# Kernel tuning notes

Hardware: AMD Instinct MI355X
Metric: run time of the kernel (lower is better)

## Reference

```python
import jax, jax.numpy as jnp
import numpy as np

EPS = 1e-12


def setup_inputs() -> dict:
    key = jax.random.key(0)
    N, C, H, W = 32, 256, 56, 56
    k1, k2, k3 = jax.random.split(key, 3)
    x = jax.random.normal(k1, (N, C, H, W), dtype=jnp.float32)
    weight = 1.0 + 0.1 * jax.random.normal(k2, (C,), dtype=jnp.float32)
    bias = 0.1 * jax.random.normal(k3, (C,), dtype=jnp.float32)
    # Variable group sizes summing to C=256 (16 groups)
    gs = np.array([8, 24, 8, 16, 32, 16, 8, 8, 16, 24, 8, 16, 16, 8, 32, 16], dtype=np.int64)
    assert gs.sum() == C
    # Per-sample channel permutation expressed as row indices into x.view(N*C, H*W)
    rng = np.random.default_rng(0)
    perms = np.stack([rng.permutation(C) for _ in range(N)])  # [N, C]
    offs = np.arange(N)[:, None] * C
    indexes = (perms + offs).reshape(-1).astype(np.int64)
    inv = np.argsort(perms, axis=1)
    reverse_indexes = (inv + offs).reshape(-1).astype(np.int64)
    return {
        "x": x,
        "weight": weight,
        "bias": bias,
        "group_sizes": jnp.asarray(gs),
        "indexes": jnp.asarray(indexes),
        "reverse_indexes": jnp.asarray(reverse_indexes),
    }


def reference(x, weight, bias, group_sizes, indexes, reverse_indexes):
    N, C, H, W = x.shape
    HW = H * W
    gs = np.asarray(group_sizes)          # static group layout
    G = gs.shape[0]
    seg = jnp.asarray(np.repeat(np.arange(G), gs))  # [C] channel -> group id
    n = jnp.asarray(gs * HW, dtype=x.dtype)         # [G] elements per group

    # gather: per-sample channel permutation
    xg = x.reshape(N * C, HW)[indexes].reshape(N, C, HW)

    # per-group mean via segmented reduction over channels
    s1 = xg.sum(axis=2)                                    # [N, C]
    mu_g = jax.ops.segment_sum(s1.T, seg, num_segments=G).T / n      # [N, G]
    mu_c = mu_g[:, seg]                                    # [N, C]

    diff = xg - mu_c[:, :, None]
    s2 = (diff * diff).sum(axis=2)                         # [N, C]
    # torch.var default is unbiased -> divide by (n - 1)
    var_g = jax.ops.segment_sum(s2.T, seg, num_segments=G).T / (n - 1.0)
    ivar_c = (1.0 / jnp.sqrt(var_g + EPS))[:, seg]         # [N, C]

    out = diff * ivar_c[:, :, None] * weight[None, :, None] + bias[None, :, None]

    # scatter back to original channel order
    out = out.reshape(N * C, HW)[reverse_indexes].reshape(N, C, H, W)
    return out
```

## Files before the change

### kernel.cpp

```cpp
#include <hip/hip_runtime.h>

#define N_ 32
#define C_ 256
#define G_ 16
#define HW_ 3136
#define HW4_ 784
#define NBIN_ 8
#define BLK_ 1024
#define NWAVE_ (BLK_ / 64)
#define EPS_ 1e-12f

typedef float vf4 __attribute__((ext_vector_type(4)));

__device__ __forceinline__ int rd_int(const int* __restrict__ p, int i, bool is64) {
    return is64 ? p[2 * i] : p[i];
}

__global__ __launch_bounds__(BLK_) void vgn_fused(
    const float* __restrict__ x,
    const int*   __restrict__ indexes,
    const int*   __restrict__ group_sizes,
    const float* __restrict__ weight,
    const float* __restrict__ bias,
    float*       __restrict__ out)
{
    const bool is64 = (group_sizes[1] == 0);
    const int n   = blockIdx.x >> 3;
    const int bin = blockIdx.x & (NBIN_ - 1);
    const int tid = threadIdx.x;

    __shared__ int   sGs[G_], sPg[G_];
    __shared__ int   sOrd[G_], sLoad[NBIN_];
    __shared__ int   sGrpId[G_];
    __shared__ int   sGrpStart[G_ + 1];
    __shared__ int   sGrpCnt, sNRows;
    __shared__ int   sRowSrc[C_];
    __shared__ float sRowScale[C_], sRowShift[C_];
    __shared__ float sMu[G_], sIvar[G_];
    __shared__ float sRed[2 * NWAVE_];

    if (tid == 0) {
        int P = 0;
        for (int k = 0; k < G_; k++) {
            int g = rd_int(group_sizes, k, is64);
            sGs[k] = g; sPg[k] = P; P += g;
            sOrd[k] = k;
        }
        for (int a = 0; a < G_; a++) {
            int best = a;
            for (int b = a + 1; b < G_; b++)
                if (sGs[sOrd[b]] > sGs[sOrd[best]]) best = b;
            int t = sOrd[a]; sOrd[a] = sOrd[best]; sOrd[best] = t;
        }
        for (int b = 0; b < NBIN_; b++) sLoad[b] = 0;
        int cnt = 0, rows = 0;
        for (int a = 0; a < G_; a++) {
            int bmin = 0;
            for (int b = 1; b < NBIN_; b++) if (sLoad[b] < sLoad[bmin]) bmin = b;
            int gid = sOrd[a];
            if (bmin == bin) {
                sGrpId[cnt]    = gid;
                sGrpStart[cnt] = rows;
                rows += sGs[gid];
                cnt++;
            }
            sLoad[bmin] += sGs[gid];
        }
        sGrpStart[cnt] = rows;
        sGrpCnt = cnt;
        sNRows  = rows;
    }
    __syncthreads();

    const int nGrp  = sGrpCnt;
    const int nRows = sNRows;

    if (tid < nRows) {
        int a = 0;
        while (!(tid >= sGrpStart[a] && tid < sGrpStart[a + 1])) a++;
        int j = sPg[sGrpId[a]] + (tid - sGrpStart[a]);
        sRowSrc[tid] = rd_int(indexes, n * C_ + j, is64);
    }
    __syncthreads();

    const int wave = tid >> 6;
    const int lane = tid & 63;

    for (int a = 0; a < nGrp; a++) {
        const int r0  = sGrpStart[a];
        const int gsz = sGrpStart[a + 1] - r0;
        const int tot = gsz * HW4_;
        float s = 0.f, s2 = 0.f;
        for (int idx = tid; idx < tot; idx += BLK_) {
            int r   = idx / HW4_;
            int col = idx - r * HW4_;
            const vf4* p = (const vf4*)(x + (size_t)sRowSrc[r0 + r] * HW_);
            vf4 v = p[col];
            s += v.x + v.y + v.z + v.w;
            s2 = fmaf(v.x, v.x, s2);
            s2 = fmaf(v.y, v.y, s2);
            s2 = fmaf(v.z, v.z, s2);
            s2 = fmaf(v.w, v.w, s2);
        }
        #pragma unroll
        for (int off = 32; off > 0; off >>= 1) {
            s  += __shfl_down(s,  off);
            s2 += __shfl_down(s2, off);
        }
        if (lane == 0) { sRed[wave] = s; sRed[NWAVE_ + wave] = s2; }
        __syncthreads();
        if (tid == 0) {
            float S = 0.f, S2 = 0.f;
            for (int w = 0; w < NWAVE_; w++) { S += sRed[w]; S2 += sRed[NWAVE_ + w]; }
            float cnt = (float)gsz * (float)HW_;
            float mu  = S / cnt;
            float var = (S2 - mu * S) / (cnt - 1.0f);
            sMu[a]   = mu;
            sIvar[a] = rsqrtf(var + EPS_);
        }
        __syncthreads();
    }

    if (tid < nRows) {
        int a = 0;
        while (!(tid >= sGrpStart[a] && tid < sGrpStart[a + 1])) a++;
        int j = sPg[sGrpId[a]] + (tid - sGrpStart[a]);
        float sc = sIvar[a] * weight[j];
        sRowScale[tid] = sc;
        sRowShift[tid] = fmaf(-sMu[a], sc, bias[j]);
    }
    __syncthreads();

    const int tot = nRows * HW4_;
    for (int idx = tid; idx < tot; idx += BLK_) {
        int r   = idx / HW4_;
        int col = idx - r * HW4_;
        const size_t base = (size_t)sRowSrc[r] * HW4_;
        vf4 v = ((const vf4*)x)[base + col];
        float sc = sRowScale[r], sh = sRowShift[r];
        vf4 o;
        o.x = fmaf(v.x, sc, sh);
        o.y = fmaf(v.y, sc, sh);
        o.z = fmaf(v.z, sc, sh);
        o.w = fmaf(v.w, sc, sh);
        __builtin_nontemporal_store(o, (vf4*)out + base + col);
    }
}

extern "C" void kernel_launch(void* const* d_in, const int* in_sizes, int n_in,
                              void* d_out, int out_size, void* d_ws, size_t ws_size,
                              hipStream_t stream) {
    const float* x           = (const float*)d_in[0];
    const float* weight      = (const float*)d_in[1];
    const float* bias        = (const float*)d_in[2];
    const int*   group_sizes = (const int*)  d_in[3];
    const int*   indexes     = (const int*)  d_in[4];

    dim3 grid(N_ * NBIN_), block(BLK_);
    vgn_fused<<<grid, block, 0, stream>>>(x, indexes, group_sizes,
                                          weight, bias, (float*)d_out);
}
```

Before: 216.3 us.

## Assign rows to half-wave teams and reduce per row instead of per group

Each 32-lane team now owns whole rows in both the statistics and normalize passes, using fixed-trip unrolled loops over the 784 vec4 columns. This removes the per-element integer division and the two block-wide barriers per group. Per-row partial sums are written to shared memory and a few threads combine them per group after a single barrier. The trade-off is less even load balance when nRows is not a multiple of 32, and a 16-lane tail that leaves half the lanes idle.

Result: no change. 214.6 us (-0.8%).

```diff
diff --git a/kernel.cpp b/kernel.cpp
--- a/kernel.cpp
+++ b/kernel.cpp
@@ -7,7 +7,6 @@
 #define HW4_ 784
 #define NBIN_ 8
 #define BLK_ 1024
-#define NWAVE_ (BLK_ / 64)
 #define EPS_ 1e-12f
 
 typedef float vf4 __attribute__((ext_vector_type(4)));
@@ -35,9 +34,9 @@
     __shared__ int   sGrpStart[G_ + 1];
     __shared__ int   sGrpCnt, sNRows;
     __shared__ int   sRowSrc[C_];
+    __shared__ float sRowS[C_], sRowS2[C_];
     __shared__ float sRowScale[C_], sRowShift[C_];
     __shared__ float sMu[G_], sIvar[G_];
-    __shared__ float sRed[2 * NWAVE_];
 
     if (tid == 0) {
         int P = 0;
@@ -77,53 +76,59 @@
 
     if (tid < nRows) {
         int a = 0;
-        while (!(tid >= sGrpStart[a] && tid < sGrpStart[a + 1])) a++;
+        while (tid >= sGrpStart[a + 1]) a++;
         int j = sPg[sGrpId[a]] + (tid - sGrpStart[a]);
         sRowSrc[tid] = rd_int(indexes, n * C_ + j, is64);
     }
     __syncthreads();
 
-    const int wave = tid >> 6;
-    const int lane = tid & 63;
+    const int rowT   = tid >> 5;
+    const int lane32 = tid & 31;
 
-    for (int a = 0; a < nGrp; a++) {
-        const int r0  = sGrpStart[a];
-        const int gsz = sGrpStart[a + 1] - r0;
-        const int tot = gsz * HW4_;
+    for (int r = rowT; r < nRows; r += 32) {
+        const vf4* p4 = (const vf4*)(x + (size_t)sRowSrc[r] * HW_);
         float s = 0.f, s2 = 0.f;
-        for (int idx = tid; idx < tot; idx += BLK_) {
-            int r   = idx / HW4_;
-            int col = idx - r * HW4_;
-            const vf4* p = (const vf4*)(x + (size_t)sRowSrc[r0 + r] * HW_);
-            vf4 v = p[col];
-            s += v.x + v.y + v.z + v.w;
-            s2 = fmaf(v.x, v.x, s2);
-            s2 = fmaf(v.y, v.y, s2);
-            s2 = fmaf(v.z, v.z, s2);
-            s2 = fmaf(v.w, v.w, s2);
+        #pragma unroll 8
+        for (int it = 0; it < 24; ++it) {
+            vf4 v = p4[lane32 + (it << 5)];
+            s  += v.x + v.y + v.z + v.w;
+            s2  = fmaf(v.x, v.x, s2);
+            s2  = fmaf(v.y, v.y, s2);
+            s2  = fmaf(v.z, v.z, s2);
+            s2  = fmaf(v.w, v.w, s2);
+        }
+        if (lane32 < 16) {
+            vf4 v = p4[768 + lane32];
+            s  += v.x + v.y + v.z + v.w;
+            s2  = fmaf(v.x, v.x, s2);
+            s2  = fmaf(v.y, v.y, s2);
+            s2  = fmaf(v.z, v.z, s2);
+            s2  = fmaf(v.w, v.w, s2);
         }
         #pragma unroll
-        for (int off = 32; off > 0; off >>= 1) {
+        for (int off = 16; off > 0; off >>= 1) {
             s  += __shfl_down(s,  off);
             s2 += __shfl_down(s2, off);
         }
-        if (lane == 0) { sRed[wave] = s; sRed[NWAVE_ + wave] = s2; }
-        __syncthreads();
-        if (tid == 0) {
-            float S = 0.f, S2 = 0.f;
-            for (int w = 0; w < NWAVE_; w++) { S += sRed[w]; S2 += sRed[NWAVE_ + w]; }
-            float cnt = (float)gsz * (float)HW_;
-            float mu  = S / cnt;
-            float var = (S2 - mu * S) / (cnt - 1.0f);
-            sMu[a]   = mu;
-            sIvar[a] = rsqrtf(var + EPS_);
-        }
-        __syncthreads();
+        if (lane32 == 0) { sRowS[r] = s; sRowS2[r] = s2; }
     }
+    __syncthreads();
+
+    if (tid < nGrp) {
+        float S = 0.f, S2 = 0.f;
+        const int r0 = sGrpStart[tid], r1 = sGrpStart[tid + 1];
+        for (int r = r0; r < r1; r++) { S += sRowS[r]; S2 += sRowS2[r]; }
+        const float cnt = (float)(r1 - r0) * (float)HW_;
+        const float mu  = S / cnt;
+        const float var = (S2 - mu * S) / (cnt - 1.0f);
+        sMu[tid]   = mu;
+        sIvar[tid] = rsqrtf(var + EPS_);
+    }
+    __syncthreads();
 
     if (tid < nRows) {
         int a = 0;
-        while (!(tid >= sGrpStart[a] && tid < sGrpStart[a + 1])) a++;
+        while (tid >= sGrpStart[a + 1]) a++;
         int j = sPg[sGrpId[a]] + (tid - sGrpStart[a]);
         float sc = sIvar[a] * weight[j];
         sRowScale[tid] = sc;
@@ -131,19 +136,32 @@
     }
     __syncthreads();
 
-    const int tot = nRows * HW4_;
-    for (int idx = tid; idx < tot; idx += BLK_) {
-        int r   = idx / HW4_;
-        int col = idx - r * HW4_;
+    for (int r = rowT; r < nRows; r += 32) {
         const size_t base = (size_t)sRowSrc[r] * HW4_;
-        vf4 v = ((const vf4*)x)[base + col];
-        float sc = sRowScale[r], sh = sRowShift[r];
-        vf4 o;
-        o.x = fmaf(v.x, sc, sh);
-        o.y = fmaf(v.y, sc, sh);
-        o.z = fmaf(v.z, sc, sh);
-        o.w = fmaf(v.w, sc, sh);
-        __builtin_nontemporal_store(o, (vf4*)out + base + col);
+        const vf4* p4 = (const vf4*)x + base;
+        vf4*       o4 = (vf4*)out     + base;
+        const float sc = sRowScale[r], sh = sRowShift[r];
+        #pragma unroll 8
+        for (int it = 0; it < 24; ++it) {
+            const int i = lane32 + (it << 5);
+            vf4 v = p4[i];
+            vf4 o;
+            o.x = fmaf(v.x, sc, sh);
+            o.y = fmaf(v.y, sc, sh);
+            o.z = fmaf(v.z, sc, sh);
+            o.w = fmaf(v.w, sc, sh);
+            __builtin_nontemporal_store(o, o4 + i);
+        }
+        if (lane32 < 16) {
+            const int i = 768 + lane32;
+            vf4 v = p4[i];
+            vf4 o;
+            o.x = fmaf(v.x, sc, sh);
+            o.y = fmaf(v.y, sc, sh);
+            o.z = fmaf(v.z, sc, sh);
+            o.w = fmaf(v.w, sc, sh);
+            __builtin_nontemporal_store(o, o4 + i);
+        }
     }
 }
 
```

## Split fused group-norm into per-row reduce and normalize kernels

Applied to the files above, without the earlier changes.

Replaces the single fused kernel, which used 256 large blocks each handling a bin of groups, with two kernels over 4096 small blocks of two rows each. The first kernel writes per-row sum and sum-of-squares to workspace. The second combines those per group with a warp shuffle and applies the affine transform. The aim is far more parallelism and less serialized group looping. In exchange, x is read twice from memory rather than partly from cache, and there is an extra launch and a dependency through workspace.

After: 202.3 us. 6.5% less time.

```diff
diff --git a/kernel.cpp b/kernel.cpp
--- a/kernel.cpp
+++ b/kernel.cpp
@@ -5,145 +5,152 @@
 #define G_ 16
 #define HW_ 3136
 #define HW4_ 784
-#define NBIN_ 8
-#define BLK_ 1024
-#define NWAVE_ (BLK_ / 64)
 #define EPS_ 1e-12f
 
 typedef float vf4 __attribute__((ext_vector_type(4)));
+typedef float vf2 __attribute__((ext_vector_type(2)));
 
 __device__ __forceinline__ int rd_int(const int* __restrict__ p, int i, bool is64) {
     return is64 ? p[2 * i] : p[i];
 }
 
-__global__ __launch_bounds__(BLK_) void vgn_fused(
+__device__ __forceinline__ void acc4(const vf4 v, float& s, float& s2) {
+    s += v.x + v.y + v.z + v.w;
+    s2 = fmaf(v.x, v.x, s2);
+    s2 = fmaf(v.y, v.y, s2);
+    s2 = fmaf(v.z, v.z, s2);
+    s2 = fmaf(v.w, v.w, s2);
+}
+
+__device__ __forceinline__ vf4 aff(const vf4 v, float sc, float sh) {
+    vf4 r;
+    r.x = fmaf(v.x, sc, sh);
+    r.y = fmaf(v.y, sc, sh);
+    r.z = fmaf(v.z, sc, sh);
+    r.w = fmaf(v.w, sc, sh);
+    return r;
+}
+
+
+__global__ __launch_bounds__(256, 8) void vgn_reduce(
+    const float* __restrict__ x,
+    const int*   __restrict__ indexes,
+    const int*   __restrict__ group_sizes,
+    float*       __restrict__ rsums)
+{
+    const bool is64 = (group_sizes[1] == 0);
+    const int t  = threadIdx.x;
+    const int r0 = blockIdx.x * 2;
+
+    const int src0 = rd_int(indexes, r0,     is64);
+    const int src1 = rd_int(indexes, r0 + 1, is64);
+    const vf4* p0 = (const vf4*)x + (size_t)src0 * HW4_;
+    const vf4* p1 = (const vf4*)x + (size_t)src1 * HW4_;
+
+    vf4 a0 = p0[t], b0 = p0[t + 256], c0 = p0[t + 512];
+    vf4 a1 = p1[t], b1 = p1[t + 256], c1 = p1[t + 512];
+
+    float sA = 0.f, qA = 0.f, sB = 0.f, qB = 0.f;
+    if (t < 16) {
+        vf4 d0 = p0[768 + t];
+        vf4 d1 = p1[768 + t];
+        acc4(d0, sA, qA);
+        acc4(d1, sB, qB);
+    }
+    acc4(a0, sA, qA); acc4(b0, sA, qA); acc4(c0, sA, qA);
+    acc4(a1, sB, qB); acc4(b1, sB, qB); acc4(c1, sB, qB);
+
+    #pragma unroll
+    for (int off = 32; off > 0; off >>= 1) {
+        sA += __shfl_down(sA, off);
+        qA += __shfl_down(qA, off);
+        sB += __shfl_down(sB, off);
+        qB += __shfl_down(qB, off);
+    }
+
+    __shared__ float red[4][4];
+    if ((t & 63) == 0) {
+        const int w = t >> 6;
+        red[w][0] = sA; red[w][1] = qA; red[w][2] = sB; red[w][3] = qB;
+    }
+    __syncthreads();
+    if (t < 4)
+        rsums[r0 * 2 + t] = red[0][t] + red[1][t] + red[2][t] + red[3][t];
+}
+
+__global__ __launch_bounds__(256, 8) void vgn_norm(
     const float* __restrict__ x,
     const int*   __restrict__ indexes,
     const int*   __restrict__ group_sizes,
     const float* __restrict__ weight,
     const float* __restrict__ bias,
+    const float* __restrict__ rsums,
     float*       __restrict__ out)
 {
     const bool is64 = (group_sizes[1] == 0);
-    const int n   = blockIdx.x >> 3;
-    const int bin = blockIdx.x & (NBIN_ - 1);
-    const int tid = threadIdx.x;
+    const int t  = threadIdx.x;
+    const int r0 = blockIdx.x * 2;
+    const int n  = r0 >> 8;
 
-    __shared__ int   sGs[G_], sPg[G_];
-    __shared__ int   sOrd[G_], sLoad[NBIN_];
-    __shared__ int   sGrpId[G_];
-    __shared__ int   sGrpStart[G_ + 1];
-    __shared__ int   sGrpCnt, sNRows;
-    __shared__ int   sRowSrc[C_];
-    __shared__ float sRowScale[C_], sRowShift[C_];
-    __shared__ float sMu[G_], sIvar[G_];
-    __shared__ float sRed[2 * NWAVE_];
+    const int src0 = rd_int(indexes, r0,     is64);
+    const int src1 = rd_int(indexes, r0 + 1, is64);
+    const vf4* p0 = (const vf4*)x + (size_t)src0 * HW4_;
+    const vf4* p1 = (const vf4*)x + (size_t)src1 * HW4_;
+    vf4* o0 = (vf4*)out + (size_t)src0 * HW4_;
+    vf4* o1 = (vf4*)out + (size_t)src1 * HW4_;
 
-    if (tid == 0) {
-        int P = 0;
+    vf4 a0 = p0[t], b0 = p0[t + 256], c0 = p0[t + 512];
+    vf4 a1 = p1[t], b1 = p1[t + 256], c1 = p1[t + 512];
+    vf4 d0, d1;
+    const bool tail = (t < 16);
+    if (tail) { d0 = p0[768 + t]; d1 = p1[768 + t]; }
+
+    __shared__ float sScale[2], sShift[2];
+    if (t < 64) {
+        const int half = t >> 5;
+        const int l    = t & 31;
+        const int j    = (r0 + half) & 255;
+        int g = 0, P = 0, Pg = 0;
+        #pragma unroll
         for (int k = 0; k < G_; k++) {
-            int g = rd_int(group_sizes, k, is64);
-            sGs[k] = g; sPg[k] = P; P += g;
-            sOrd[k] = k;
+            P += rd_int(group_sizes, k, is64);
+            if (j >= P) { g++; Pg = P; }
         }
-        for (int a = 0; a < G_; a++) {
-            int best = a;
-            for (int b = a + 1; b < G_; b++)
-                if (sGs[sOrd[b]] > sGs[sOrd[best]]) best = b;
-            int t = sOrd[a]; sOrd[a] = sOrd[best]; sOrd[best] = t;
+        const int gsz = rd_int(group_sizes, g, is64);
+        float a = 0.f, b = 0.f;
+        if (l < gsz) {
+            const vf2 pr = ((const vf2*)rsums)[n * C_ + Pg + l];
+            a = pr.x; b = pr.y;
         }
-        for (int b = 0; b < NBIN_; b++) sLoad[b] = 0;
-        int cnt = 0, rows = 0;
-        for (int a = 0; a < G_; a++) {
-            int bmin = 0;
-            for (int b = 1; b < NBIN_; b++) if (sLoad[b] < sLoad[bmin]) bmin = b;
-            int gid = sOrd[a];
-            if (bmin == bin) {
-                sGrpId[cnt]    = gid;
-                sGrpStart[cnt] = rows;
-                rows += sGs[gid];
-                cnt++;
-            }
-            sLoad[bmin] += sGs[gid];
+        #pragma unroll
+        for (int off = 16; off > 0; off >>= 1) {
+            a += __shfl_down(a, off, 32);
+            b += __shfl_down(b, off, 32);
         }
-        sGrpStart[cnt] = rows;
-        sGrpCnt = cnt;
-        sNRows  = rows;
+        if (l == 0) {
+            const float cnt = (float)gsz * (float)HW_;
+            const float mu  = a / cnt;
+            const float var = (b - mu * a) / (cnt - 1.0f);
+            const float ivr = rsqrtf(var + EPS_);
+            const float sc  = ivr * weight[j];
+            sScale[half] = sc;
+            sShift[half] = fmaf(-mu, sc, bias[j]);
+        }
     }
     __syncthreads();
 
-    const int nGrp  = sGrpCnt;
-    const int nRows = sNRows;
+    const float sc0 = sScale[0], sh0 = sShift[0];
+    const float sc1 = sScale[1], sh1 = sShift[1];
 
-    if (tid < nRows) {
-        int a = 0;
-        while (!(tid >= sGrpStart[a] && tid < sGrpStart[a + 1])) a++;
-        int j = sPg[sGrpId[a]] + (tid - sGrpStart[a]);
-        sRowSrc[tid] = rd_int(indexes, n * C_ + j, is64);
-    }
-    __syncthreads();
-
-    const int wave = tid >> 6;
-    const int lane = tid & 63;
-
-    for (int a = 0; a < nGrp; a++) {
-        const int r0  = sGrpStart[a];
-        const int gsz = sGrpStart[a + 1] - r0;
-        const int tot = gsz * HW4_;
-        float s = 0.f, s2 = 0.f;
-        for (int idx = tid; idx < tot; idx += BLK_) {
-            int r   = idx / HW4_;
-            int col = idx - r * HW4_;
-            const vf4* p = (const vf4*)(x + (size_t)sRowSrc[r0 + r] * HW_);
-            vf4 v = p[col];
-            s += v.x + v.y + v.z + v.w;
-            s2 = fmaf(v.x, v.x, s2);
-            s2 = fmaf(v.y, v.y, s2);
-            s2 = fmaf(v.z, v.z, s2);
-            s2 = fmaf(v.w, v.w, s2);
-        }
-        #pragma unroll
-        for (int off = 32; off > 0; off >>= 1) {
-            s  += __shfl_down(s,  off);
-            s2 += __shfl_down(s2, off);
-        }
-        if (lane == 0) { sRed[wave] = s; sRed[NWAVE_ + wave] = s2; }
-        __syncthreads();
-        if (tid == 0) {
-            float S = 0.f, S2 = 0.f;
-            for (int w = 0; w < NWAVE_; w++) { S += sRed[w]; S2 += sRed[NWAVE_ + w]; }
-            float cnt = (float)gsz * (float)HW_;
-            float mu  = S / cnt;
-            float var = (S2 - mu * S) / (cnt - 1.0f);
-            sMu[a]   = mu;
-            sIvar[a] = rsqrtf(var + EPS_);
-        }
-        __syncthreads();
-    }
-
-    if (tid < nRows) {
-        int a = 0;
-        while (!(tid >= sGrpStart[a] && tid < sGrpStart[a + 1])) a++;
-        int j = sPg[sGrpId[a]] + (tid - sGrpStart[a]);
-        float sc = sIvar[a] * weight[j];
-        sRowScale[tid] = sc;
-        sRowShift[tid] = fmaf(-sMu[a], sc, bias[j]);
-    }
-    __syncthreads();
-
-    const int tot = nRows * HW4_;
-    for (int idx = tid; idx < tot; idx += BLK_) {
-        int r   = idx / HW4_;
-        int col = idx - r * HW4_;
-        const size_t base = (size_t)sRowSrc[r] * HW4_;
-        vf4 v = ((const vf4*)x)[base + col];
-        float sc = sRowScale[r], sh = sRowShift[r];
-        vf4 o;
-        o.x = fmaf(v.x, sc, sh);
-        o.y = fmaf(v.y, sc, sh);
-        o.z = fmaf(v.z, sc, sh);
-        o.w = fmaf(v.w, sc, sh);
-        __builtin_nontemporal_store(o, (vf4*)out + base + col);
+    __builtin_nontemporal_store(aff(a0, sc0, sh0), o0 + t);
+    __builtin_nontemporal_store(aff(b0, sc0, sh0), o0 + t + 256);
+    __builtin_nontemporal_store(aff(c0, sc0, sh0), o0 + t + 512);
+    __builtin_nontemporal_store(aff(a1, sc1, sh1), o1 + t);
+    __builtin_nontemporal_store(aff(b1, sc1, sh1), o1 + t + 256);
+    __builtin_nontemporal_store(aff(c1, sc1, sh1), o1 + t + 512);
+    if (tail) {
+        __builtin_nontemporal_store(aff(d0, sc0, sh0), o0 + 768 + t);
+        __builtin_nontemporal_store(aff(d1, sc1, sh1), o1 + 768 + t);
     }
 }
 
@@ -156,7 +163,10 @@
     const int*   group_sizes = (const int*)  d_in[3];
     const int*   indexes     = (const int*)  d_in[4];
 
-    dim3 grid(N_ * NBIN_), block(BLK_);
-    vgn_fused<<<grid, block, 0, stream>>>(x, indexes, group_sizes,
-                                          weight, bias, (float*)d_out);
+    float* rsums = (float*)d_ws;
+
+    dim3 grid(N_ * C_ / 2), block(256);
+    vgn_reduce<<<grid, block, 0, stream>>>(x, indexes, group_sizes, rsums);
+    vgn_norm  <<<grid, block, 0, stream>>>(x, indexes, group_sizes,
+                                           weight, bias, rsums, (float*)d_out);
 }
```
